# Kernel tuning notes

Hardware: AMD Instinct MI355X
Metric: run time of the kernel (lower is better)

## Reference

```python
import jax, jax.numpy as jnp
import numpy as np

N, C = 8192, 4096
EPS = 1e-12


def setup_inputs() -> dict:
    key = jax.random.key(0)
    kx, ky = jax.random.split(key)
    act_X = jax.random.normal(kx, (N, C), dtype=jnp.float32)
    act_Y = jax.random.normal(ky, (N, C), dtype=jnp.float32)
    return {"act_X": act_X, "act_Y": act_Y}


def reference(act_X, act_Y):
    # softmax over class dim (dim=1 in the torch module)
    probs_X = jax.nn.softmax(act_X, axis=1)  # [N, C]
    probs_Y = jax.nn.softmax(act_Y, axis=1)  # [N, C]

    # approximate_entropy_cu: mean per-sample Shannon entropy (nats)
    entropy = jnp.mean(-jnp.sum(probs_X * jnp.log(probs_X + EPS), axis=1))

    # approximate_mi_cu: plug-in MI from batch-averaged joint distribution
    n = probs_X.shape[0]
    joint = jnp.einsum('nc,nd->cd', probs_X, probs_Y) / n  # [C, C]
    marg_X = jnp.mean(probs_X, axis=0)  # [C]
    marg_Y = jnp.mean(probs_Y, axis=0)  # [C]
    log_ratio = jnp.log(joint + EPS) - (jnp.log(marg_X + EPS)[:, None]
                                        + jnp.log(marg_Y + EPS)[None, :])
    mi = jnp.sum(joint * log_ratio)

    return jnp.stack([entropy, mi])  # shape [2]
```

## Files before the change

### kernel.cpp

```cpp
#include <hip/hip_runtime.h>
#include <hip/hip_bf16.h>
#include <stdint.h>

#define NROWS 8192
#define CDIM  4096
#define KDIM  8192
#define EPS   1e-12f

typedef __attribute__((ext_vector_type(8)))  int   v8i;
typedef __attribute__((ext_vector_type(4)))  int   v4i;
typedef __attribute__((ext_vector_type(4)))  float f32x4;
typedef __attribute__((ext_vector_type(2)))  float f32x2;

__device__ inline float wave_sum(float v) {
#pragma unroll
    for (int o = 32; o > 0; o >>= 1) v += __shfl_xor(v, o, 64);
    return v;
}
__device__ inline float wave_max(float v) {
#pragma unroll
    for (int o = 32; o > 0; o >>= 1) v = fmaxf(v, __shfl_xor(v, o, 64));
    return v;
}

__global__ __launch_bounds__(256) void row_quant_kernel(const float* __restrict__ X,
                                                        const float* __restrict__ Y,
                                                        unsigned char* __restrict__ QX,
                                                        unsigned char* __restrict__ QY,
                                                        float* __restrict__ entPart,
                                                        float* __restrict__ zbase) {
    const int t = threadIdx.x, lane = t & 63, wave = t >> 6;
    if (blockIdx.x == 0 && blockIdx.y == 0) {
        for (int i = t; i < 8256; i += 256) zbase[i] = 0.f;
    }
    const int row = blockIdx.x * 4 + wave;
    const bool isY = blockIdx.y != 0;
    const float4* s4 = (const float4*)((isY ? Y : X) + (size_t)row * CDIM);
    unsigned int* dst = (unsigned int*)((isY ? QY : QX) + (size_t)row * CDIM);
    float4 v[16];
#pragma unroll
    for (int i = 0; i < 16; i++) v[i] = s4[i * 64 + lane];
    float m = -3.0e38f;
#pragma unroll
    for (int i = 0; i < 16; i++)
        m = fmaxf(m, fmaxf(fmaxf(v[i].x, v[i].y), fmaxf(v[i].z, v[i].w)));
    m = wave_max(m);
    float Z = 0.f, S = 0.f;
#pragma unroll
    for (int i = 0; i < 16; i++) {
        float e;
        e = __expf(v[i].x - m); Z += e; S += e * v[i].x; v[i].x = e;
        e = __expf(v[i].y - m); Z += e; S += e * v[i].y; v[i].y = e;
        e = __expf(v[i].z - m); Z += e; S += e * v[i].z; v[i].z = e;
        e = __expf(v[i].w - m); Z += e; S += e * v[i].w; v[i].w = e;
    }
    Z = wave_sum(Z); S = wave_sum(S);
    __shared__ float sent[4];
    if (lane == 0) sent[wave] = m + __logf(Z) - S / Z;
    const float sc = 512.0f / Z;
#pragma unroll
    for (int i = 0; i < 16; i++) {
        unsigned int w0 = (unsigned int)__builtin_amdgcn_cvt_pk_fp8_f32(
            v[i].x * sc, v[i].y * sc, 0, false);
        w0 = (unsigned int)__builtin_amdgcn_cvt_pk_fp8_f32(
            v[i].z * sc, v[i].w * sc, (int)w0, true);
        dst[i * 64 + lane] = w0;
    }
    __syncthreads();
    if (t == 0 && !isY)
        entPart[blockIdx.x] = sent[0] + sent[1] + sent[2] + sent[3];
}

__global__ __launch_bounds__(256) void transpose_marg_kernel(
        const unsigned char* __restrict__ QX, const unsigned char* __restrict__ QY,
        unsigned char* __restrict__ QXT, unsigned char* __restrict__ QYT,
        float* __restrict__ margX, float* __restrict__ margY) {
    const bool isY = blockIdx.z != 0;
    const unsigned char* __restrict__ Q = isY ? QY : QX;
    unsigned char* __restrict__ QT = isY ? QYT : QXT;
    float* __restrict__ marg = isY ? margY : margX;

    __shared__ __align__(16) unsigned char tile[128 * 128];
    __shared__ float smarg[128];
    const int t = threadIdx.x;
    const int c0 = blockIdx.x * 128, n0 = blockIdx.y * 128;
    if (t < 128) smarg[t] = 0.f;
    __syncthreads();
    const int cq = (t & 31) * 4;
    const int nq = (t >> 5) * 16;
    const unsigned char* src = Q + (size_t)(n0 + nq) * CDIM + c0 + cq;
    unsigned int u[16];
#pragma unroll
    for (int i = 0; i < 16; i++)
        u[i] = *(const unsigned int*)(src + (size_t)i * CDIM);
#pragma unroll
    for (int j = 0; j < 4; j++) {
        const unsigned int sel = (unsigned)j | ((unsigned)(j + 4) << 8);
        unsigned int d0, d1, d2, d3;
        {
            unsigned int p01 = __builtin_amdgcn_perm(u[1], u[0], sel);
            unsigned int p23 = __builtin_amdgcn_perm(u[3], u[2], sel);
            d0 = __builtin_amdgcn_perm(p23, p01, 0x05040100u);
        }
        {
            unsigned int p01 = __builtin_amdgcn_perm(u[5], u[4], sel);
            unsigned int p23 = __builtin_amdgcn_perm(u[7], u[6], sel);
            d1 = __builtin_amdgcn_perm(p23, p01, 0x05040100u);
        }
        {
            unsigned int p01 = __builtin_amdgcn_perm(u[9], u[8], sel);
            unsigned int p23 = __builtin_amdgcn_perm(u[11], u[10], sel);
            d2 = __builtin_amdgcn_perm(p23, p01, 0x05040100u);
        }
        {
            unsigned int p01 = __builtin_amdgcn_perm(u[13], u[12], sel);
            unsigned int p23 = __builtin_amdgcn_perm(u[15], u[14], sel);
            d3 = __builtin_amdgcn_perm(p23, p01, 0x05040100u);
        }
        const int r = cq + j;
        uint4 o; o.x = d0; o.y = d1; o.z = d2; o.w = d3;
        *(uint4*)&tile[r * 128 + ((((nq >> 4) ^ ((r >> 2) & 7))) << 4)] = o;
        float s = 0.f;
        f32x2 a;
        a = __builtin_amdgcn_cvt_pk_f32_fp8((int)d0, false); s += a.x + a.y;
        a = __builtin_amdgcn_cvt_pk_f32_fp8((int)d0, true);  s += a.x + a.y;
        a = __builtin_amdgcn_cvt_pk_f32_fp8((int)d1, false); s += a.x + a.y;
        a = __builtin_amdgcn_cvt_pk_f32_fp8((int)d1, true);  s += a.x + a.y;
        a = __builtin_amdgcn_cvt_pk_f32_fp8((int)d2, false); s += a.x + a.y;
        a = __builtin_amdgcn_cvt_pk_f32_fp8((int)d2, true);  s += a.x + a.y;
        a = __builtin_amdgcn_cvt_pk_f32_fp8((int)d3, false); s += a.x + a.y;
        a = __builtin_amdgcn_cvt_pk_f32_fp8((int)d3, true);  s += a.x + a.y;
        atomicAdd(&smarg[r], s);
    }
    __syncthreads();
#pragma unroll
    for (int p = 0; p < 4; p++) {
        const int r = p * 32 + (t >> 3);
        const int k = t & 7;
        uint4 o = *(const uint4*)&tile[r * 128 + (((k ^ ((r >> 2) & 7))) << 4)];
        *(uint4*)(QT + (size_t)(c0 + r) * KDIM + n0 + k * 16) = o;
    }
    if (t < 128) atomicAdd(&marg[c0 + t], smarg[t]);
}

#define GLD16(g, l)                                                                   \
    __builtin_amdgcn_global_load_lds((const __attribute__((address_space(1))) unsigned int*)(g), \
                                     (__attribute__((address_space(3))) unsigned int*)(l), 16, 0, 0)

#define BUFSZ 65536
#define BOFS  32768

__global__ __launch_bounds__(512, 2) void gemm_mi_kernel(const unsigned char* __restrict__ A,
                                                         const unsigned char* __restrict__ B,
                                                         float* __restrict__ S_out) {
    __shared__ __align__(16) unsigned char lds[131072];
    const int t = threadIdx.x;
    const int lane = t & 63, wave = t >> 6;
    const int m0 = blockIdx.x * 256, n0 = blockIdx.y * 256;

    const int srow = wave * 32 + (lane >> 3);
    const int gcol = ((lane & 7) ^ (lane >> 3)) * 16;
    const unsigned char* ga = A + (size_t)(m0 + srow) * KDIM + gcol;
    const unsigned char* gb = B + (size_t)(n0 + srow) * KDIM + gcol;
    const int loff = wave * 4096 + lane * 16;

    const int wm = (wave >> 2) * 128, wn = (wave & 3) * 64;
    const int fr = lane & 15, quad = lane >> 4, sw = fr & 7;
    const int off0 = ((2 * quad)     ^ sw) * 16;
    const int off1 = ((2 * quad + 1) ^ sw) * 16;

    f32x4 acc[8][4];
#pragma unroll
    for (int i = 0; i < 8; i++)
#pragma unroll
        for (int j = 0; j < 4; j++) { acc[i][j][0] = 0.f; acc[i][j][1] = 0.f; acc[i][j][2] = 0.f; acc[i][j][3] = 0.f; }

#pragma unroll
    for (int i = 0; i < 4; i++) {
        GLD16(ga + (size_t)i * 8 * KDIM, lds + loff + i * 1024);
        GLD16(gb + (size_t)i * 8 * KDIM, lds + BOFS + loff + i * 1024);
    }

    int cur = 0;
    for (int tt = 0; tt < KDIM / 128; ++tt) {
        if (tt + 1 < KDIM / 128) {
            const int nb = (cur ^ 1) * BUFSZ;
            const int kn = (tt + 1) * 128;
#pragma unroll
            for (int i = 0; i < 4; i++) {
                GLD16(ga + (size_t)i * 8 * KDIM + kn, lds + nb + loff + i * 1024);
                GLD16(gb + (size_t)i * 8 * KDIM + kn, lds + nb + BOFS + loff + i * 1024);
            }
            asm volatile("s_waitcnt vmcnt(8)" ::: "memory");
        } else {
            asm volatile("s_waitcnt vmcnt(0)" ::: "memory");
        }
        asm volatile("s_barrier" ::: "memory");
        __builtin_amdgcn_sched_barrier(0);

        const unsigned char* base = lds + cur * BUFSZ;
        v8i bg[4];
#pragma unroll
        for (int j = 0; j < 4; j++) {
            const unsigned char* pB = base + BOFS + (wn + j * 16 + fr) * 128;
            v4i lo = *(const v4i*)(pB + off0);
            v4i hi = *(const v4i*)(pB + off1);
            bg[j][0] = lo[0]; bg[j][1] = lo[1]; bg[j][2] = lo[2]; bg[j][3] = lo[3];
            bg[j][4] = hi[0]; bg[j][5] = hi[1]; bg[j][6] = hi[2]; bg[j][7] = hi[3];
        }
        __builtin_amdgcn_s_setprio(1);
#pragma unroll
        for (int i = 0; i < 8; i++) {
            const unsigned char* pA = base + (wm + i * 16 + fr) * 128;
            v4i lo = *(const v4i*)(pA + off0);
            v4i hi = *(const v4i*)(pA + off1);
            v8i af;
            af[0] = lo[0]; af[1] = lo[1]; af[2] = lo[2]; af[3] = lo[3];
            af[4] = hi[0]; af[5] = hi[1]; af[6] = hi[2]; af[7] = hi[3];
#pragma unroll
            for (int j = 0; j < 4; j++)
                acc[i][j] = __builtin_amdgcn_mfma_scale_f32_16x16x128_f8f6f4(
                    af, bg[j], acc[i][j], 0 , 0 ,
                    0, 0x7f , 0, 0x7f );
        }
        __builtin_amdgcn_s_setprio(0);
        __builtin_amdgcn_sched_barrier(0);
        asm volatile("s_waitcnt lgkmcnt(0)" ::: "memory");
        asm volatile("s_barrier" ::: "memory");
        __builtin_amdgcn_sched_barrier(0);
        cur ^= 1;
    }

    const float invS = 4.656612873077393e-10f;
    float loc = 0.f;
#pragma unroll
    for (int i = 0; i < 8; i++)
#pragma unroll
        for (int j = 0; j < 4; j++)
#pragma unroll
            for (int r = 0; r < 4; r++) {
                float v = acc[i][j][r] * invS;
                loc += v * __logf(v + EPS);
            }
    loc = wave_sum(loc);
    __shared__ float sred[8];
    if (lane == 0) sred[wave] = loc;
    __syncthreads();
    if (t == 0) {
        float s = 0.f;
#pragma unroll
        for (int w = 0; w < 8; w++) s += sred[w];
        atomicAdd(S_out, s);
    }
}

__global__ __launch_bounds__(256) void finalize_kernel(const float* __restrict__ accums,
                                                       const float* __restrict__ entPart,
                                                       const float* __restrict__ margX,
                                                       const float* __restrict__ margY,
                                                       float* __restrict__ out) {
    const int t = threadIdx.x;
    const int lane = t & 63, w = t >> 6;
    const float invN = 1.0f / 8192.0f;
    const float invM = 1.0f / 4194304.0f;
    float sx = 0.f, sy = 0.f, se = 0.f;
    for (int c = t; c < CDIM; c += 256) {
        float mx = margX[c] * invM;
        float my = margY[c] * invM;
        sx += mx * __logf(mx + EPS);
        sy += my * __logf(my + EPS);
    }
    for (int c = t; c < 2048; c += 256) se += entPart[c];
    sx = wave_sum(sx); sy = wave_sum(sy); se = wave_sum(se);
    __shared__ float rx[4], ry[4], re[4];
    if (lane == 0) { rx[w] = sx; ry[w] = sy; re[w] = se; }
    __syncthreads();
    if (t == 0) {
        float SX = rx[0] + rx[1] + rx[2] + rx[3];
        float SY = ry[0] + ry[1] + ry[2] + ry[3];
        float SE = re[0] + re[1] + re[2] + re[3];
        out[0] = SE * invN;
        out[1] = accums[0] - SX - SY;
    }
}

extern "C" void kernel_launch(void* const* d_in, const int* in_sizes, int n_in,
                              void* d_out, int out_size, void* d_ws, size_t ws_size,
                              hipStream_t stream) {
    const float* X = (const float*)d_in[0];
    const float* Y = (const float*)d_in[1];
    char* ws = (char*)d_ws;
    unsigned char* QX  = (unsigned char*)ws;
    unsigned char* QY  = (unsigned char*)(ws + 33554432ll);
    unsigned char* QXT = (unsigned char*)(ws + 67108864ll);
    unsigned char* QYT = (unsigned char*)(ws + 100663296ll);
    float* margX = (float*)(ws + 134217728ll);
    float* margY = (float*)(ws + 134234112ll);
    float* accums = (float*)(ws + 134250496ll);
    float* entPart = (float*)(ws + 134250752ll);

    row_quant_kernel<<<dim3(2048, 2), 256, 0, stream>>>(X, Y, QX, QY, entPart, margX);
    transpose_marg_kernel<<<dim3(CDIM / 128, NROWS / 128, 2), 256, 0, stream>>>(
        QX, QY, QXT, QYT, margX, margY);
    gemm_mi_kernel<<<dim3(CDIM / 256, CDIM / 256), 512, 0, stream>>>(QXT, QYT, &accums[0]);
    finalize_kernel<<<1, 256, 0, stream>>>(accums, entPart, margX, margY, (float*)d_out);
}
```

Before: 458.0 us.

## Use 4 waves with 128x128 per-wave tiles in FP8 MI GEMM

The GEMM block drops from 8 waves to 4, and each wave now computes a 128x128 output sub-tile (8x8 MFMA tiles) instead of 128x64. This raises the ratio of MFMA work to LDS fragment loads per wave, and each thread issues twice as many global-to-LDS loads, with the wait count adjusted to match. The cost is doubled accumulator registers (256 floats per thread), which risks lower occupancy or register spills. With the 128KB LDS buffer only one block can fit per CU anyway.

Result: slower. 474.2 us (+3.5%).

```diff
diff --git a/kernel.cpp b/kernel.cpp
--- a/kernel.cpp
+++ b/kernel.cpp
@@ -150,33 +150,42 @@
 #define BUFSZ 65536
 #define BOFS  32768
 
-__global__ __launch_bounds__(512, 2) void gemm_mi_kernel(const unsigned char* __restrict__ A,
-                                                         const unsigned char* __restrict__ B,
-                                                         float* __restrict__ S_out) {
+__device__ __forceinline__ v8i pack8(const unsigned char* p, int off0, int off1) {
+    v4i lo = *(const v4i*)(p + off0);
+    v4i hi = *(const v4i*)(p + off1);
+    v8i a;
+    a[0] = lo[0]; a[1] = lo[1]; a[2] = lo[2]; a[3] = lo[3];
+    a[4] = hi[0]; a[5] = hi[1]; a[6] = hi[2]; a[7] = hi[3];
+    return a;
+}
+
+__global__ __launch_bounds__(256) void gemm_mi_kernel(const unsigned char* __restrict__ A,
+                                                      const unsigned char* __restrict__ B,
+                                                      float* __restrict__ S_out) {
     __shared__ __align__(16) unsigned char lds[131072];
     const int t = threadIdx.x;
     const int lane = t & 63, wave = t >> 6;
     const int m0 = blockIdx.x * 256, n0 = blockIdx.y * 256;
 
-    const int srow = wave * 32 + (lane >> 3);
+    const int srow = wave * 64 + (lane >> 3);
     const int gcol = ((lane & 7) ^ (lane >> 3)) * 16;
     const unsigned char* ga = A + (size_t)(m0 + srow) * KDIM + gcol;
     const unsigned char* gb = B + (size_t)(n0 + srow) * KDIM + gcol;
-    const int loff = wave * 4096 + lane * 16;
-
-    const int wm = (wave >> 2) * 128, wn = (wave & 3) * 64;
+    const int loff = wave * 8192 + lane * 16;
+
+    const int wm = (wave & 1) * 128, wn = (wave >> 1) * 128;
     const int fr = lane & 15, quad = lane >> 4, sw = fr & 7;
     const int off0 = ((2 * quad)     ^ sw) * 16;
     const int off1 = ((2 * quad + 1) ^ sw) * 16;
 
-    f32x4 acc[8][4];
+    f32x4 acc[8][8];
 #pragma unroll
     for (int i = 0; i < 8; i++)
 #pragma unroll
-        for (int j = 0; j < 4; j++) { acc[i][j][0] = 0.f; acc[i][j][1] = 0.f; acc[i][j][2] = 0.f; acc[i][j][3] = 0.f; }
-
-#pragma unroll
-    for (int i = 0; i < 4; i++) {
+        for (int j = 0; j < 8; j++) { acc[i][j][0] = 0.f; acc[i][j][1] = 0.f; acc[i][j][2] = 0.f; acc[i][j][3] = 0.f; }
+
+#pragma unroll
+    for (int i = 0; i < 8; i++) {
         GLD16(ga + (size_t)i * 8 * KDIM, lds + loff + i * 1024);
         GLD16(gb + (size_t)i * 8 * KDIM, lds + BOFS + loff + i * 1024);
     }
@@ -187,11 +196,11 @@
             const int nb = (cur ^ 1) * BUFSZ;
             const int kn = (tt + 1) * 128;
 #pragma unroll
-            for (int i = 0; i < 4; i++) {
+            for (int i = 0; i < 8; i++) {
                 GLD16(ga + (size_t)i * 8 * KDIM + kn, lds + nb + loff + i * 1024);
                 GLD16(gb + (size_t)i * 8 * KDIM + kn, lds + nb + BOFS + loff + i * 1024);
             }
-            asm volatile("s_waitcnt vmcnt(8)" ::: "memory");
+            asm volatile("s_waitcnt vmcnt(16)" ::: "memory");
         } else {
             asm volatile("s_waitcnt vmcnt(0)" ::: "memory");
         }
@@ -199,26 +208,16 @@
         __builtin_amdgcn_sched_barrier(0);
 
         const unsigned char* base = lds + cur * BUFSZ;
-        v8i bg[4];
-#pragma unroll
-        for (int j = 0; j < 4; j++) {
-            const unsigned char* pB = base + BOFS + (wn + j * 16 + fr) * 128;
-            v4i lo = *(const v4i*)(pB + off0);
-            v4i hi = *(const v4i*)(pB + off1);
-            bg[j][0] = lo[0]; bg[j][1] = lo[1]; bg[j][2] = lo[2]; bg[j][3] = lo[3];
-            bg[j][4] = hi[0]; bg[j][5] = hi[1]; bg[j][6] = hi[2]; bg[j][7] = hi[3];
-        }
+        v8i bg[8];
+#pragma unroll
+        for (int j = 0; j < 8; j++)
+            bg[j] = pack8(base + BOFS + (wn + j * 16 + fr) * 128, off0, off1);
         __builtin_amdgcn_s_setprio(1);
 #pragma unroll
         for (int i = 0; i < 8; i++) {
-            const unsigned char* pA = base + (wm + i * 16 + fr) * 128;
-            v4i lo = *(const v4i*)(pA + off0);
-            v4i hi = *(const v4i*)(pA + off1);
-            v8i af;
-            af[0] = lo[0]; af[1] = lo[1]; af[2] = lo[2]; af[3] = lo[3];
-            af[4] = hi[0]; af[5] = hi[1]; af[6] = hi[2]; af[7] = hi[3];
-#pragma unroll
-            for (int j = 0; j < 4; j++)
+            v8i af = pack8(base + (wm + i * 16 + fr) * 128, off0, off1);
+#pragma unroll
+            for (int j = 0; j < 8; j++)
                 acc[i][j] = __builtin_amdgcn_mfma_scale_f32_16x16x128_f8f6f4(
                     af, bg[j], acc[i][j], 0 , 0 ,
                     0, 0x7f , 0, 0x7f );
@@ -236,22 +235,17 @@
 #pragma unroll
     for (int i = 0; i < 8; i++)
 #pragma unroll
-        for (int j = 0; j < 4; j++)
+        for (int j = 0; j < 8; j++)
 #pragma unroll
             for (int r = 0; r < 4; r++) {
                 float v = acc[i][j][r] * invS;
                 loc += v * __logf(v + EPS);
             }
     loc = wave_sum(loc);
-    __shared__ float sred[8];
+    __shared__ float sred[4];
     if (lane == 0) sred[wave] = loc;
     __syncthreads();
-    if (t == 0) {
-        float s = 0.f;
-#pragma unroll
-        for (int w = 0; w < 8; w++) s += sred[w];
-        atomicAdd(S_out, s);
-    }
+    if (t == 0) atomicAdd(S_out, sred[0] + sred[1] + sred[2] + sred[3]);
 }
 
 __global__ __launch_bounds__(256) void finalize_kernel(const float* __restrict__ accums,
@@ -302,6 +296,6 @@
     row_quant_kernel<<<dim3(2048, 2), 256, 0, stream>>>(X, Y, QX, QY, entPart, margX);
     transpose_marg_kernel<<<dim3(CDIM / 128, NROWS / 128, 2), 256, 0, stream>>>(
         QX, QY, QXT, QYT, margX, margY);
-    gemm_mi_kernel<<<dim3(CDIM / 256, CDIM / 256), 512, 0, stream>>>(QXT, QYT, &accums[0]);
+    gemm_mi_kernel<<<dim3(CDIM / 256, CDIM / 256), 256, 0, stream>>>(QXT, QYT, &accums[0]);
     finalize_kernel<<<1, 256, 0, stream>>>(accums, entPart, margX, margY, (float*)d_out);
 }
```
